# Kernel optimization log

Hardware: AMD Instinct MI355X
Metric: run time of the kernel (lower is better)

The kernel has to match this reference:

```python
import jax, jax.numpy as jnp
import numpy as np

TAU1, TAU2, TSCALE = 30.0, 5.0, 6.0   # tau1 > tau2, in frame units (hz=None)
B, T_OUT = 1000, 20000                # neurons x output frames


def _biexp_kernel():
    # exact replica of SpikeToCalcium.set_double_exp
    r = TAU1 / TAU2
    d = TAU1 - TAU2
    scale = np.power(r, -TAU2 / d) - np.power(r, -TAU1 / d)
    t = np.arange(1.0, TAU1 * TSCALE + 2.0, dtype=np.float32)  # 181 taps
    e1 = np.exp(-t / TAU1)
    e2 = np.exp(-t / TAU2)
    return ((e1 - e2) / scale).astype(np.float32)


def setup_inputs() -> dict:
    key = jax.random.key(0)
    kernel = jnp.asarray(_biexp_kernel())           # (181,)
    Kt = kernel.shape[0]
    u = jax.random.normal(key, (B, T_OUT + Kt - 1), dtype=jnp.float32)  # (1000, 20180)
    return {"u": u, "kernel": kernel}


def reference(u, kernel):
    # Original: K.conv1d(u[..., None], kernel[::-1, None, None], 1, 'valid')
    # keras conv1d is cross-correlation; reversing the kernel makes it a true
    # causal FIR convolution. lax.conv_general_dilated is also cross-correlation,
    # so we pass the reversed kernel identically.
    rhs = kernel[::-1][None, None, :]               # (O=1, I=1, K)
    lhs = u[:, None, :]                             # (B, C=1, T_in)
    out = jax.lax.conv_general_dilated(
        lhs, rhs, window_strides=(1,), padding='VALID',
        dimension_numbers=('NCH', 'OIH', 'NCH'))
    return out[:, 0, :]                             # (B, T_in - K + 1)
```

## Files before the change

### kernel.cpp

```cpp
#include <hip/hip_runtime.h>
#include <math.h>


namespace {
constexpr int kB    = 1000;
constexpr int kT    = 20000;
constexpr int kInW  = kT + 180;
constexpr int W     = 180;
constexpr int L     = 836;
constexpr int SEGS  = 24;
constexpr int NTASK = SEGS * kB;
constexpr int NBLK  = 2048;
constexpr int NWAVE = NBLK * 4;
}

struct Coefs {
  float r1e[8], r2e[8];
  float s1c[6], s2c[6];
  float r1_512;
  float A1, A1d, A2;
};

__global__ __launch_bounds__(256, 8)
void biexp_iir_scan(const float* __restrict__ u, float* __restrict__ out, Coefs cf) {
  const int lane = threadIdx.x & 63;

  const int lbid = (blockIdx.x & 7) * (NBLK >> 3) + (blockIdx.x >> 3);
  const int w    = (lbid << 2) | (threadIdx.x >> 6);

  float r1l = 1.f, r2l = 1.f;
  #pragma unroll
  for (int i = 0; i < 6; ++i) {
    r1l *= (lane & (1 << i)) ? cf.s1c[i] : 1.f;
    r2l *= (lane & (1 << i)) ? cf.s2c[i] : 1.f;
  }

  auto load_task = [&](int t, float4& a0, float4& a1, float4& b0, float4& b1) {
    const int row = t / SEGS;
    const int n0  = (t - row * SEGS) * L;
    const float* ur = u + (size_t)row * kInW;
    int c0 = n0 + 8 * lane;
    c0 = c0 < (kInW - 8) ? c0 : (kInW - 8);
    int c1 = n0 + 512 + 8 * lane;
    c1 = c1 < (kInW - 8) ? c1 : (kInW - 8);
    a0 = *(const float4*)(ur + c0);
    a1 = *(const float4*)(ur + c0 + 4);
    b0 = *(const float4*)(ur + c1);
    b1 = *(const float4*)(ur + c1 + 4);
  };

  auto compute_store = [&](int t, const float4& qa0, const float4& qa1,
                                  const float4& qb0, const float4& qb1) {
    const int row  = t / SEGS;
    const int n0   = (t - row * SEGS) * L;
    const int nend = (n0 + L < kT) ? n0 + L : kT;
    const int lim  = nend - n0 + W;
    float* outr = out + (size_t)row * kT;

    float C1 = 0.f, C2 = 0.f;
    float pw[8];
    #pragma unroll
    for (int j = 0; j < 8; ++j) pw[j] = 0.f;

    #pragma unroll
    for (int c = 0; c < 2; ++c) {
      const float4& qa = c ? qb0 : qa0;
      const float4& qb = c ? qb1 : qa1;
      const float ux[8] = {qa.x, qa.y, qa.z, qa.w, qb.x, qb.y, qb.z, qb.w};

      float p1[8], p2[8];
      p1[0] = ux[0]; p2[0] = ux[0];
      #pragma unroll
      for (int j = 1; j < 8; ++j) {
        p1[j] = fmaf(cf.r1e[1], p1[j-1], ux[j]);
        p2[j] = fmaf(cf.r2e[1], p2[j-1], ux[j]);
      }

      float S1 = p1[7], S2 = p2[7], t_;
      t_ = __shfl_up(S1, 1);  S1 = lane >= 1  ? fmaf(cf.s1c[0], t_, S1) : S1;
      t_ = __shfl_up(S2, 1);  S2 = lane >= 1  ? fmaf(cf.s2c[0], t_, S2) : S2;
      t_ = __shfl_up(S1, 2);  S1 = lane >= 2  ? fmaf(cf.s1c[1], t_, S1) : S1;
      t_ = __shfl_up(S2, 2);  S2 = lane >= 2  ? fmaf(cf.s2c[1], t_, S2) : S2;
      t_ = __shfl_up(S1, 4);  S1 = lane >= 4  ? fmaf(cf.s1c[2], t_, S1) : S1;
      t_ = __shfl_up(S2, 4);  S2 = lane >= 4  ? fmaf(cf.s2c[2], t_, S2) : S2;
      t_ = __shfl_up(S1, 8);  S1 = lane >= 8  ? fmaf(cf.s1c[3], t_, S1) : S1;
      t_ = __shfl_up(S2, 8);  S2 = lane >= 8  ? fmaf(cf.s2c[3], t_, S2) : S2;
      t_ = __shfl_up(S1, 16); S1 = lane >= 16 ? fmaf(cf.s1c[4], t_, S1) : S1;
      t_ = __shfl_up(S1, 32); S1 = lane >= 32 ? fmaf(cf.s1c[5], t_, S1) : S1;

      float X1 = __shfl_up(S1, 1); X1 = (lane == 0) ? 0.f : X1;
      float X2 = __shfl_up(S2, 1); X2 = (lane == 0) ? 0.f : X2;
      const float H1 = cf.r1e[1] * fmaf(r1l, C1, X1);
      const float H2 = cf.r2e[1] * fmaf(r2l, C2, X2);

      float s1[8], s2[8];
      #pragma unroll
      for (int j = 0; j < 8; ++j) {
        s1[j] = fmaf(cf.r1e[j], H1, p1[j]);
        s2[j] = fmaf(cf.r2e[j], H2, p2[j]);
      }
      C1 = fmaf(cf.r1_512, C1, __shfl(S1, 63));
      C2 = __shfl(S2, 63);

      float y[8];
      #pragma unroll
      for (int j = 0; j < 8; ++j) {
        const int slot = (j < 5) ? j + 3 : j - 5;
        const int rot  = (j < 5) ? 23 : 22;
        const float z  = (lane <= 63 - rot) ? s1[slot] : pw[slot];
        const float d  = __shfl(z, (lane - rot) & 63);
        y[j] = fmaf(-cf.A2, s2[j], fmaf(-cf.A1d, d, cf.A1 * s1[j]));
      }
      #pragma unroll
      for (int j = 0; j < 8; ++j) pw[j] = s1[j];

      const int off0 = (c << 9) + 8 * lane;
      if (off0 >= W && off0 < lim) {
        float4 v; v.x = y[0]; v.y = y[1]; v.z = y[2]; v.w = y[3];
        *(float4*)(outr + (n0 - W + off0)) = v;
      }
      if (off0 + 4 >= W && off0 + 4 < lim) {
        float4 v; v.x = y[4]; v.y = y[5]; v.z = y[6]; v.w = y[7];
        *(float4*)(outr + (n0 - W + off0 + 4)) = v;
      }
    }
  };

  int t = w;
  float4 A0, A1v, B0, B1;
  load_task(t, A0, A1v, B0, B1);

  #pragma unroll
  for (int i = 0; i < 3; ++i) {
    if (i > 0 && t >= NTASK) break;
    const int tn = t + NWAVE;
    float4 P0, P1, P2, P3;
    if (i < 2) {
      const int tl = (tn < NTASK) ? tn : t;
      load_task(tl, P0, P1, P2, P3);
      __builtin_amdgcn_sched_barrier(0);
    }
    compute_store(t, A0, A1v, B0, B1);
    if (i < 2) { A0 = P0; A1v = P1; B0 = P2; B1 = P3; t = tn; }
  }
}

extern "C" void kernel_launch(void* const* d_in, const int* in_sizes, int n_in,
                              void* d_out, int out_size, void* d_ws, size_t ws_size,
                              hipStream_t stream) {
  const float* u = (const float*)d_in[0];
  float* out = (float*)d_out;

  const double r1 = exp(-1.0 / 30.0);
  const double r2 = exp(-1.0 / 5.0);
  const double scale = pow(6.0, -5.0 / 25.0) - pow(6.0, -30.0 / 25.0);

  Coefs cf;
  for (int j = 0; j < 8; ++j) {
    cf.r1e[j] = (float)pow(r1, (double)j);
    cf.r2e[j] = (float)pow(r2, (double)j);
  }
  for (int i = 0; i < 6; ++i) {
    cf.s1c[i] = (float)pow(r1, (double)(8 << i));
    cf.s2c[i] = (float)pow(r2, (double)(8 << i));
  }
  cf.r1_512 = (float)pow(r1, 512.0);
  cf.A1  = (float)(r1 / scale);
  cf.A1d = (float)(pow(r1, 182.0) / scale);
  cf.A2  = (float)(r2 / scale);

  hipLaunchKernelGGL(biexp_iir_scan, dim3(NBLK), dim3(256, 1, 1), 0, stream,
                     u, out, cf);
}
```

Before: 176.2 us.

## Assign contiguous segment triples per wave with depth-2 prefetch pipeline

Replaces the strided grid-wide task loop with a fixed mapping in which each wave handles three consecutive segments of one row, so row and segment indices come from shifts instead of divisions. Loads for two segments are issued up front, and the third is loaded after the first is computed, deepening the prefetch. The grid size now matches the work exactly (2000 blocks), which drops the tail checks and the block swizzle. The costs are more live registers for the double buffer and the loss of the interleaved block ordering.

```diff
diff --git a/kernel.cpp b/kernel.cpp
--- a/kernel.cpp
+++ b/kernel.cpp
@@ -9,9 +9,9 @@
 constexpr int W     = 180;
 constexpr int L     = 836;
 constexpr int SEGS  = 24;
-constexpr int NTASK = SEGS * kB;
-constexpr int NBLK  = 2048;
-constexpr int NWAVE = NBLK * 4;
+constexpr int K     = 3;
+constexpr int NWAVE = kB * SEGS / K;
+constexpr int NBLK  = NWAVE / 4;
 }
 
 struct Coefs {
@@ -24,9 +24,12 @@
 __global__ __launch_bounds__(256, 8)
 void biexp_iir_scan(const float* __restrict__ u, float* __restrict__ out, Coefs cf) {
   const int lane = threadIdx.x & 63;
+  const int w    = (blockIdx.x << 2) | (threadIdx.x >> 6);
+  const int row  = w >> 3;
+  const int seg0 = (w & 7) * K;
 
-  const int lbid = (blockIdx.x & 7) * (NBLK >> 3) + (blockIdx.x >> 3);
-  const int w    = (lbid << 2) | (threadIdx.x >> 6);
+  const float* ur = u + (size_t)row * kInW;
+  float* outr = out + (size_t)row * kT;
 
   float r1l = 1.f, r2l = 1.f;
   #pragma unroll
@@ -35,10 +38,7 @@
     r2l *= (lane & (1 << i)) ? cf.s2c[i] : 1.f;
   }
 
-  auto load_task = [&](int t, float4& a0, float4& a1, float4& b0, float4& b1) {
-    const int row = t / SEGS;
-    const int n0  = (t - row * SEGS) * L;
-    const float* ur = u + (size_t)row * kInW;
+  auto load_tile = [&](int n0, float4& a0, float4& a1, float4& b0, float4& b1) {
     int c0 = n0 + 8 * lane;
     c0 = c0 < (kInW - 8) ? c0 : (kInW - 8);
     int c1 = n0 + 512 + 8 * lane;
@@ -49,13 +49,10 @@
     b1 = *(const float4*)(ur + c1 + 4);
   };
 
-  auto compute_store = [&](int t, const float4& qa0, const float4& qa1,
-                                  const float4& qb0, const float4& qb1) {
-    const int row  = t / SEGS;
-    const int n0   = (t - row * SEGS) * L;
+  auto seg_compute = [&](int n0, const float4& qa0, const float4& qa1,
+                                 const float4& qb0, const float4& qb1) {
     const int nend = (n0 + L < kT) ? n0 + L : kT;
     const int lim  = nend - n0 + W;
-    float* outr = out + (size_t)row * kT;
 
     float C1 = 0.f, C2 = 0.f;
     float pw[8];
@@ -126,23 +123,19 @@
     }
   };
 
-  int t = w;
-  float4 A0, A1v, B0, B1;
-  load_task(t, A0, A1v, B0, B1);
+  const int n0_0 = (seg0    ) * L;
+  const int n0_1 = (seg0 + 1) * L;
+  const int n0_2 = (seg0 + 2) * L;
 
-  #pragma unroll
-  for (int i = 0; i < 3; ++i) {
-    if (i > 0 && t >= NTASK) break;
-    const int tn = t + NWAVE;
-    float4 P0, P1, P2, P3;
-    if (i < 2) {
-      const int tl = (tn < NTASK) ? tn : t;
-      load_task(tl, P0, P1, P2, P3);
-      __builtin_amdgcn_sched_barrier(0);
-    }
-    compute_store(t, A0, A1v, B0, B1);
-    if (i < 2) { A0 = P0; A1v = P1; B0 = P2; B1 = P3; t = tn; }
-  }
+  float4 A0, A1v, A2v, A3;
+  float4 B0, B1, B2, B3;
+  load_tile(n0_0, A0, A1v, A2v, A3);
+  load_tile(n0_1, B0, B1, B2, B3);
+
+  seg_compute(n0_0, A0, A1v, A2v, A3);
+  load_tile(n0_2, A0, A1v, A2v, A3);
+  seg_compute(n0_1, B0, B1, B2, B3);
+  seg_compute(n0_2, A0, A1v, A2v, A3);
 }
 
 extern "C" void kernel_launch(void* const* d_in, const int* in_sizes, int n_in,
```

After: 173.3 us. No clear change (-1.7%).
